# Optimization experiments

Measured on AMD Instinct MI355X. Metric: run time of the kernel, lower is better.

## Reference

```python
import jax, jax.numpy as jnp
import numpy as np

DIM = 1024
HEADS = 16

def setup_inputs() -> dict:
    key = jax.random.key(0)
    k1, k2, k3, k4 = jax.random.split(key, 4)
    x = jax.random.normal(k1, (2, 2048, DIM), dtype=jnp.float32)
    # torch Linear weights are [out_features, in_features]
    w_qkv = jax.random.normal(k2, (3 * DIM, DIM), dtype=jnp.float32) * (DIM ** -0.5)
    w_out = jax.random.normal(k3, (DIM, DIM), dtype=jnp.float32) * (DIM ** -0.5)
    b_out = jax.random.normal(k4, (DIM,), dtype=jnp.float32) * 0.01
    return {"x": x, "w_qkv": w_qkv, "w_out": w_out, "b_out": b_out}

def reference(x, w_qkv, w_out, b_out):
    b, n, dim = x.shape
    h = HEADS
    d = dim // h
    scale = dim ** -0.5  # NOTE: full dim, faithful to source
    qkv = x @ w_qkv.T                       # [b, n, 3*dim]
    qkv = qkv.reshape(b, n, 3, h, d)        # split (qkv h d)
    q, k, v = (qkv[:, :, i].transpose(0, 2, 1, 3) for i in range(3))  # [b, h, n, d]
    scores = jnp.einsum('bhid,bhjd->bhij', q, k) * scale
    weights = jax.nn.softmax(scores, axis=-1)
    out = jnp.einsum('bhij,bhjd->bhid', weights, v)  # [b, h, n, d]
    out = out.transpose(0, 2, 1, 3).reshape(b, n, dim)
    return out @ w_out.T + b_out
```

## Files before the change

kernel.cpp:

```cpp
#include <hip/hip_runtime.h>

#define DIM   1024
#define HEADS 16
#define NSEQ  2048
#define BATCH 2

typedef unsigned short u16;
typedef unsigned long long u64;
typedef __attribute__((ext_vector_type(8))) short bf16x8;
typedef __attribute__((ext_vector_type(8))) _Float16 f16x8;
typedef __attribute__((ext_vector_type(2))) __fp16 pkh2;
typedef __attribute__((ext_vector_type(4))) float f32x4;
typedef __attribute__((ext_vector_type(16))) float f32x16;

__device__ __forceinline__ u16 f2b(float f) {
  union { float f; unsigned u; } v; v.f = f;
  unsigned r = (v.u + 0x7fffu + ((v.u >> 16) & 1u)) >> 16;
  return (u16)r;
}

__device__ __forceinline__ u16 f2h(float f) {
  _Float16 h = (_Float16)f;
  return __builtin_bit_cast(u16, h);
}

__device__ __forceinline__ void g2l16(const u16* g, u16* l) {
  __builtin_amdgcn_global_load_lds(
      (const __attribute__((address_space(1))) void*)g,
      (__attribute__((address_space(3))) void*)l, 16, 0, 0);
}

__global__ void cvt_bf16(const float* __restrict__ src, u16* __restrict__ dst,
                         int n4, int sc4, float s) {
  int i = blockIdx.x * blockDim.x + threadIdx.x;
  if (i < n4) {
    float4 f = ((const float4*)src)[i];
    float m = (i < sc4) ? s : 1.0f;
    union { u16 s[4]; u64 ll; } o;
    o.s[0] = f2b(f.x * m); o.s[1] = f2b(f.y * m);
    o.s[2] = f2b(f.z * m); o.s[3] = f2b(f.w * m);
    ((u64*)dst)[i] = o.ll;
  }
}

__global__ __launch_bounds__(256, 2)
void gemm_bt(const u16* __restrict__ A, const u16* __restrict__ Bt,
             void* __restrict__ C, const float* __restrict__ bias,
             int M, int Nc, int K, int mode) {
  __shared__ u16 As[128 * 64];
  __shared__ u16 Bs[128 * 64];
  const int tid  = threadIdx.x;
  const int wave = tid >> 6, lane = tid & 63;
  const int l15  = lane & 15, quad = lane >> 4;
  const int m0 = blockIdx.y * 128, n0 = blockIdx.x * 128;
  const int wm = (wave >> 1) * 64, wn = (wave & 1) * 64;
  const int rb = wave * 32;

  f32x4 acc[4][4] = {};

  for (int kt = 0; kt < K; kt += 64) {
#pragma unroll
    for (int c = 0; c < 4; ++c) {
      int r  = rb + c * 8 + (lane >> 3);
      int ck = (lane & 7) ^ (r & 7);
      g2l16(A  + (size_t)(m0 + r) * K + kt + ck * 8, &As[(rb + c * 8) * 64]);
      g2l16(Bt + (size_t)(n0 + r) * K + kt + ck * 8, &Bs[(rb + c * 8) * 64]);
    }
    __syncthreads();
#pragma unroll
    for (int ks = 0; ks < 2; ++ks) {
      bf16x8 a[4], b[4];
      int ch = ks * 4 + quad;
#pragma unroll
      for (int i = 0; i < 4; ++i) {
        int ra  = wm + i * 16 + l15;
        a[i] = *(const bf16x8*)&As[ra * 64 + ((ch ^ (ra & 7)) << 3)];
        int rb2 = wn + i * 16 + l15;
        b[i] = *(const bf16x8*)&Bs[rb2 * 64 + ((ch ^ (rb2 & 7)) << 3)];
      }
#pragma unroll
      for (int i = 0; i < 4; ++i)
#pragma unroll
        for (int j = 0; j < 4; ++j)
          acc[i][j] = __builtin_amdgcn_mfma_f32_16x16x32_bf16(a[i], b[j], acc[i][j], 0, 0, 0);
    }
    __syncthreads();
  }

  const int as_f16 = (mode == 2) && (n0 >= 2048);
#pragma unroll
  for (int i = 0; i < 4; ++i)
#pragma unroll
    for (int j = 0; j < 4; ++j) {
      int row = m0 + wm + i * 16 + quad * 4;
      int col = n0 + wn + j * 16 + l15;
#pragma unroll
      for (int r = 0; r < 4; ++r) {
        float v = acc[i][j][r];
        if (mode == 0) ((float*)C)[(size_t)(row + r) * Nc + col] = v + bias[col];
        else ((u16*)C)[(size_t)(row + r) * Nc + col] = as_f16 ? f2h(v) : f2b(v);
      }
    }
}

__global__ __launch_bounds__(256, 2)
void attn(const u16* __restrict__ qkv, u16* __restrict__ outp) {
  __shared__ u16 Ks[2][128 * 64];
  __shared__ u16 Vts[2][64 * 128];
  const int tid  = threadIdx.x;
  const int wave = tid >> 6, lane = tid & 63;
  const int l31  = lane & 31, h = lane >> 5;
  const int b = blockIdx.x >> 4, hd = blockIdx.x & 15;
  const int q0 = blockIdx.y * 128;
  const u16* base = qkv + (size_t)b * NSEQ * 3072;
  const int qoff = hd * 64, koff = DIM + hd * 64, voff = 2 * DIM + hd * 64;
  const int dc = tid & 7, j0l = (tid >> 3) * 4;
  const int vchunk = (j0l >> 4) * 2 + ((j0l >> 2) & 1);
  const int vboff  = 4 * ((j0l >> 3) & 1);

  union V4 { uint4 q; u16 s[8]; };
  union PA { unsigned w[4]; f16x8 f; };

#pragma unroll
  for (int c = 0; c < 4; ++c) {
    int bse = wave * 32 + c * 8;
    g2l16(base + (size_t)(q0 + bse + (lane >> 3)) * 3072 + qoff + (((lane & 7) ^ ((lane >> 3) & 7)) << 3),
          &Ks[0][bse * 64]);
  }
  __syncthreads();
  bf16x8 qf[4];
  {
    int qr = wave * 32 + l31;
#pragma unroll
    for (int kd = 0; kd < 4; ++kd)
      qf[kd] = *(const bf16x8*)&Ks[0][qr * 64 + (((kd * 2 + h) ^ (qr & 7)) << 3)];
  }
  __syncthreads();

  V4 vr[4];
#pragma unroll
  for (int c = 0; c < 4; ++c) {
    int bse = wave * 32 + c * 8;
    g2l16(base + (size_t)(bse + (lane >> 3)) * 3072 + koff + (((lane & 7) ^ ((lane >> 3) & 7)) << 3),
          &Ks[0][bse * 64]);
  }
#pragma unroll
  for (int e = 0; e < 4; ++e)
    vr[e].q = *(const uint4*)(base + (size_t)(j0l + e) * 3072 + voff + dc * 8);
#pragma unroll
  for (int u = 0; u < 8; ++u) {
    int d = dc * 8 + u;
    unsigned w0 = (unsigned)vr[0].s[u] | ((unsigned)vr[1].s[u] << 16);
    unsigned w1 = (unsigned)vr[2].s[u] | ((unsigned)vr[3].s[u] << 16);
    *(u64*)&Vts[0][d * 128 + ((vchunk ^ ((d + (d >> 3)) & 15)) << 3) + vboff] =
        (u64)w0 | ((u64)w1 << 32);
  }
  __syncthreads();

  float lrun = 0.0f;
  f32x16 oacc[2] = {};

  for (int t = 0; t < 16; ++t) {
    const int pbuf = t & 1;
    if (t < 15) {
      const int j0n = (t + 1) * 128;
#pragma unroll
      for (int c = 0; c < 4; ++c) {
        int bse = wave * 32 + c * 8;
        g2l16(base + (size_t)(j0n + bse + (lane >> 3)) * 3072 + koff + (((lane & 7) ^ ((lane >> 3) & 7)) << 3),
              &Ks[pbuf ^ 1][bse * 64]);
      }
#pragma unroll
      for (int e = 0; e < 4; ++e)
        vr[e].q = *(const uint4*)(base + (size_t)(j0n + j0l + e) * 3072 + voff + dc * 8);
    }

    f32x16 sc[4] = {};
#pragma unroll
    for (int kd = 0; kd < 4; ++kd) {
      bf16x8 kb[4];
#pragma unroll
      for (int ni = 0; ni < 4; ++ni) {
        int kr = ni * 32 + l31;
        kb[ni] = *(const bf16x8*)&Ks[pbuf][kr * 64 + (((kd * 2 + h) ^ (kr & 7)) << 3)];
      }
#pragma unroll
      for (int ni = 0; ni < 4; ++ni)
        sc[ni] = __builtin_amdgcn_mfma_f32_32x32x16_bf16(kb[ni], qf[kd], sc[ni], 0, 0, 0);
    }

    PA pa[8];
#pragma unroll
    for (int ni = 0; ni < 4; ++ni) {
      f32x16 p;
#pragma unroll
      for (int r = 0; r < 16; ++r) p[r] = __builtin_amdgcn_exp2f(sc[ni][r]);
      float s0 = (p[0] + p[1]) + (p[2] + p[3]);
      float s1 = (p[4] + p[5]) + (p[6] + p[7]);
      float s2 = (p[8] + p[9]) + (p[10] + p[11]);
      float s3 = (p[12] + p[13]) + (p[14] + p[15]);
      lrun += (s0 + s1) + (s2 + s3);
#pragma unroll
      for (int ks2 = 0; ks2 < 2; ++ks2)
#pragma unroll
        for (int i = 0; i < 4; ++i) {
          pkh2 t = __builtin_amdgcn_cvt_pkrtz(p[8 * ks2 + 2 * i], p[8 * ks2 + 2 * i + 1]);
          pa[2 * ni + ks2].w[i] = __builtin_bit_cast(unsigned, t);
        }
    }

#pragma unroll
    for (int f = 0; f < 8; ++f) {
      f16x8 vb[2];
#pragma unroll
      for (int nd = 0; nd < 2; ++nd) {
        int d = nd * 32 + l31;
        vb[nd] = *(const f16x8*)&Vts[pbuf][d * 128 + (((2 * f + h) ^ ((d + (d >> 3)) & 15)) << 3)];
      }
#pragma unroll
      for (int nd = 0; nd < 2; ++nd)
        oacc[nd] = __builtin_amdgcn_mfma_f32_32x32x16_f16(pa[f].f, vb[nd], oacc[nd], 0, 0, 0);
    }

    if (t < 15) {
#pragma unroll
      for (int u = 0; u < 8; ++u) {
        int d = dc * 8 + u;
        unsigned w0 = (unsigned)vr[0].s[u] | ((unsigned)vr[1].s[u] << 16);
        unsigned w1 = (unsigned)vr[2].s[u] | ((unsigned)vr[3].s[u] << 16);
        *(u64*)&Vts[pbuf ^ 1][d * 128 + ((vchunk ^ ((d + (d >> 3)) & 15)) << 3) + vboff] =
            (u64)w0 | ((u64)w1 << 32);
      }
    }
    __syncthreads();
  }

  float linv = 1.0f / (lrun + __shfl_xor(lrun, 32, 64));
#pragma unroll
  for (int r = 0; r < 16; ++r) {
    int rowloc = (r & 3) + 8 * (r >> 2) + 4 * h;
    float lb = __shfl(linv, rowloc, 64);
    int row = q0 + wave * 32 + rowloc;
#pragma unroll
    for (int nd = 0; nd < 2; ++nd)
      outp[((size_t)b * NSEQ + row) * DIM + hd * 64 + nd * 32 + l31] = f2b(oacc[nd][r] * lb);
  }
}

extern "C" void kernel_launch(void* const* d_in, const int* in_sizes, int n_in,
                              void* d_out, int out_size, void* d_ws, size_t ws_size,
                              hipStream_t stream) {
  const float* x     = (const float*)d_in[0];
  const float* w_qkv = (const float*)d_in[1];
  const float* w_out = (const float*)d_in[2];
  const float* b_out = (const float*)d_in[3];
  float* outp = (float*)d_out;

  u16* xb    = (u16*)d_ws;
  u16* wqkvb = xb    + (size_t)4096 * 1024;
  u16* woutb = wqkvb + (size_t)3072 * 1024;
  u16* qkvb  = woutb + (size_t)1024 * 1024;
  u16* attnb = qkvb  + (size_t)4096 * 3072;

  const float C2 = 0.03125f * 1.44269504088896340736f;

  cvt_bf16<<<4096 * 1024 / 4 / 256, 256, 0, stream>>>(x,     xb,    4096 * 1024 / 4, 0, 1.0f);
  cvt_bf16<<<3072 * 1024 / 4 / 256, 256, 0, stream>>>(w_qkv, wqkvb, 3072 * 1024 / 4,
                                                      1024 * 1024 / 4, C2);
  cvt_bf16<<<1024 * 1024 / 4 / 256, 256, 0, stream>>>(w_out, woutb, 1024 * 1024 / 4, 0, 1.0f);

  gemm_bt<<<dim3(24, 32), 256, 0, stream>>>(xb, wqkvb, qkvb, nullptr, 4096, 3072, 1024, 2);
  attn<<<dim3(32, 16), 256, 0, stream>>>(qkvb, attnb);
  gemm_bt<<<dim3(8, 32), 256, 0, stream>>>(attnb, woutb, outp, b_out, 4096, 1024, 1024, 0);
}
```

Baseline: 206.9 us.

## Pre-transpose V into a global fp16 buffer and stream it directly into attention

A new kernel transposes V into a [b*h, 64, N] fp16 layout in global memory, converting it from the bf16 that the QKV GEMM now always writes. The attention kernel drops its LDS V staging, register transposes and writes, and instead loads the V operands for the PV MFMAs directly from the transposed global buffer. The score computation is also reordered into two halves of 64 keys to reduce live registers. This trades an extra kernel launch and global round-trip, plus uncached per-iteration global loads in the inner loop, for less LDS traffic and less shuffle work. V also picks up an extra rounding step, since it is now quantised to bf16 before being converted to fp16.

```diff
diff --git a/kernel.cpp b/kernel.cpp
--- a/kernel.cpp
+++ b/kernel.cpp
@@ -87,7 +87,6 @@
     __syncthreads();
   }
 
-  const int as_f16 = (mode == 2) && (n0 >= 2048);
 #pragma unroll
   for (int i = 0; i < 4; ++i)
 #pragma unroll
@@ -98,27 +97,52 @@
       for (int r = 0; r < 4; ++r) {
         float v = acc[i][j][r];
         if (mode == 0) ((float*)C)[(size_t)(row + r) * Nc + col] = v + bias[col];
-        else ((u16*)C)[(size_t)(row + r) * Nc + col] = as_f16 ? f2h(v) : f2b(v);
-      }
-    }
+        else ((u16*)C)[(size_t)(row + r) * Nc + col] = f2b(v);
+      }
+    }
+}
+
+__global__ __launch_bounds__(256)
+void vt_kernel(const u16* __restrict__ qkv, u16* __restrict__ vt) {
+  __shared__ u16 T[64][136];
+  const int tid = threadIdx.x;
+  const int bh = blockIdx.x, b = bh >> 4, h = bh & 15;
+  const int j0 = blockIdx.y * 128;
+  const u16* src = qkv + (size_t)b * NSEQ * 3072 + 2 * DIM + h * 64;
+#pragma unroll
+  for (int p = 0; p < 8; ++p) {
+    int jl = p * 16 + (tid >> 4);
+    int d0 = (tid & 15) * 4;
+    u64 v = *(const u64*)&src[(size_t)(j0 + jl) * 3072 + d0];
+#pragma unroll
+    for (int e = 0; e < 4; ++e) {
+      unsigned bf = (unsigned)((v >> (16 * e)) & 0xFFFFu) << 16;
+      T[d0 + e][jl] = f2h(__builtin_bit_cast(float, bf));
+    }
+  }
+  __syncthreads();
+  const int d = tid >> 2, g = tid & 3;
+  u16* dst = vt + ((size_t)bh * 64 + d) * NSEQ + j0 + g * 32;
+#pragma unroll
+  for (int c = 0; c < 4; ++c)
+    *(uint4*)&dst[c * 8] = *(const uint4*)&T[d][g * 32 + c * 8];
 }
 
 __global__ __launch_bounds__(256, 2)
-void attn(const u16* __restrict__ qkv, u16* __restrict__ outp) {
+void attn(const u16* __restrict__ qkv, const u16* __restrict__ vt,
+          u16* __restrict__ outp) {
   __shared__ u16 Ks[2][128 * 64];
-  __shared__ u16 Vts[2][64 * 128];
   const int tid  = threadIdx.x;
   const int wave = tid >> 6, lane = tid & 63;
   const int l31  = lane & 31, h = lane >> 5;
-  const int b = blockIdx.x >> 4, hd = blockIdx.x & 15;
+  const int bh = blockIdx.x, b = bh >> 4, hd = bh & 15;
   const int q0 = blockIdx.y * 128;
   const u16* base = qkv + (size_t)b * NSEQ * 3072;
-  const int qoff = hd * 64, koff = DIM + hd * 64, voff = 2 * DIM + hd * 64;
-  const int dc = tid & 7, j0l = (tid >> 3) * 4;
-  const int vchunk = (j0l >> 4) * 2 + ((j0l >> 2) & 1);
-  const int vboff  = 4 * ((j0l >> 3) & 1);
-
-  union V4 { uint4 q; u16 s[8]; };
+  const int qoff = hd * 64, koff = DIM + hd * 64;
+  const u16* vrow0 = vt + ((size_t)bh * 64 + l31) * NSEQ;
+  const u16* vrow1 = vrow0 + (size_t)32 * NSEQ;
+
+  union VF { u64 d[2]; f16x8 v; };
   union PA { unsigned w[4]; f16x8 f; };
 
 #pragma unroll
@@ -137,24 +161,12 @@
   }
   __syncthreads();
 
-  V4 vr[4];
 #pragma unroll
   for (int c = 0; c < 4; ++c) {
     int bse = wave * 32 + c * 8;
     g2l16(base + (size_t)(bse + (lane >> 3)) * 3072 + koff + (((lane & 7) ^ ((lane >> 3) & 7)) << 3),
           &Ks[0][bse * 64]);
   }
-#pragma unroll
-  for (int e = 0; e < 4; ++e)
-    vr[e].q = *(const uint4*)(base + (size_t)(j0l + e) * 3072 + voff + dc * 8);
-#pragma unroll
-  for (int u = 0; u < 8; ++u) {
-    int d = dc * 8 + u;
-    unsigned w0 = (unsigned)vr[0].s[u] | ((unsigned)vr[1].s[u] << 16);
-    unsigned w1 = (unsigned)vr[2].s[u] | ((unsigned)vr[3].s[u] << 16);
-    *(u64*)&Vts[0][d * 128 + ((vchunk ^ ((d + (d >> 3)) & 15)) << 3) + vboff] =
-        (u64)w0 | ((u64)w1 << 32);
-  }
   __syncthreads();
 
   float lrun = 0.0f;
@@ -170,67 +182,53 @@
         g2l16(base + (size_t)(j0n + bse + (lane >> 3)) * 3072 + koff + (((lane & 7) ^ ((lane >> 3) & 7)) << 3),
               &Ks[pbuf ^ 1][bse * 64]);
       }
-#pragma unroll
-      for (int e = 0; e < 4; ++e)
-        vr[e].q = *(const uint4*)(base + (size_t)(j0n + j0l + e) * 3072 + voff + dc * 8);
-    }
-
-    f32x16 sc[4] = {};
-#pragma unroll
-    for (int kd = 0; kd < 4; ++kd) {
-      bf16x8 kb[4];
-#pragma unroll
-      for (int ni = 0; ni < 4; ++ni) {
-        int kr = ni * 32 + l31;
-        kb[ni] = *(const bf16x8*)&Ks[pbuf][kr * 64 + (((kd * 2 + h) ^ (kr & 7)) << 3)];
-      }
-#pragma unroll
-      for (int ni = 0; ni < 4; ++ni)
-        sc[ni] = __builtin_amdgcn_mfma_f32_32x32x16_bf16(kb[ni], qf[kd], sc[ni], 0, 0, 0);
     }
 
     PA pa[8];
 #pragma unroll
-    for (int ni = 0; ni < 4; ++ni) {
-      f32x16 p;
-#pragma unroll
-      for (int r = 0; r < 16; ++r) p[r] = __builtin_amdgcn_exp2f(sc[ni][r]);
-      float s0 = (p[0] + p[1]) + (p[2] + p[3]);
-      float s1 = (p[4] + p[5]) + (p[6] + p[7]);
-      float s2 = (p[8] + p[9]) + (p[10] + p[11]);
-      float s3 = (p[12] + p[13]) + (p[14] + p[15]);
-      lrun += (s0 + s1) + (s2 + s3);
-#pragma unroll
-      for (int ks2 = 0; ks2 < 2; ++ks2)
-#pragma unroll
-        for (int i = 0; i < 4; ++i) {
-          pkh2 t = __builtin_amdgcn_cvt_pkrtz(p[8 * ks2 + 2 * i], p[8 * ks2 + 2 * i + 1]);
-          pa[2 * ni + ks2].w[i] = __builtin_bit_cast(unsigned, t);
-        }
-    }
-
+    for (int half = 0; half < 2; ++half) {
+      f32x16 s0 = {}, s1 = {};
+      const int kr0 = half * 64 + l31, kr1 = kr0 + 32;
+#pragma unroll
+      for (int kd = 0; kd < 4; ++kd) {
+        int ch = kd * 2 + h;
+        bf16x8 kb0 = *(const bf16x8*)&Ks[pbuf][kr0 * 64 + ((ch ^ (kr0 & 7)) << 3)];
+        bf16x8 kb1 = *(const bf16x8*)&Ks[pbuf][kr1 * 64 + ((ch ^ (kr1 & 7)) << 3)];
+        s0 = __builtin_amdgcn_mfma_f32_32x32x16_bf16(kb0, qf[kd], s0, 0, 0, 0);
+        s1 = __builtin_amdgcn_mfma_f32_32x32x16_bf16(kb1, qf[kd], s1, 0, 0, 0);
+      }
+#pragma unroll
+      for (int u = 0; u < 2; ++u) {
+        const f32x16& su = u ? s1 : s0;
+        f32x16 p;
+#pragma unroll
+        for (int r = 0; r < 16; ++r) p[r] = __builtin_amdgcn_exp2f(su[r]);
+        float a0 = (p[0] + p[1]) + (p[2] + p[3]);
+        float a1 = (p[4] + p[5]) + (p[6] + p[7]);
+        float a2 = (p[8] + p[9]) + (p[10] + p[11]);
+        float a3 = (p[12] + p[13]) + (p[14] + p[15]);
+        lrun += (a0 + a1) + (a2 + a3);
+#pragma unroll
+        for (int ks2 = 0; ks2 < 2; ++ks2)
+#pragma unroll
+          for (int i = 0; i < 4; ++i) {
+            pkh2 t2 = __builtin_amdgcn_cvt_pkrtz(p[8 * ks2 + 2 * i], p[8 * ks2 + 2 * i + 1]);
+            pa[4 * half + 2 * u + ks2].w[i] = __builtin_bit_cast(unsigned, t2);
+          }
+      }
+    }
+
+    const int j0 = t * 128;
 #pragma unroll
     for (int f = 0; f < 8; ++f) {
-      f16x8 vb[2];
-#pragma unroll
-      for (int nd = 0; nd < 2; ++nd) {
-        int d = nd * 32 + l31;
-        vb[nd] = *(const f16x8*)&Vts[pbuf][d * 128 + (((2 * f + h) ^ ((d + (d >> 3)) & 15)) << 3)];
-      }
-#pragma unroll
-      for (int nd = 0; nd < 2; ++nd)
-        oacc[nd] = __builtin_amdgcn_mfma_f32_32x32x16_f16(pa[f].f, vb[nd], oacc[nd], 0, 0, 0);
-    }
-
-    if (t < 15) {
-#pragma unroll
-      for (int u = 0; u < 8; ++u) {
-        int d = dc * 8 + u;
-        unsigned w0 = (unsigned)vr[0].s[u] | ((unsigned)vr[1].s[u] << 16);
-        unsigned w1 = (unsigned)vr[2].s[u] | ((unsigned)vr[3].s[u] << 16);
-        *(u64*)&Vts[pbuf ^ 1][d * 128 + ((vchunk ^ ((d + (d >> 3)) & 15)) << 3) + vboff] =
-            (u64)w0 | ((u64)w1 << 32);
-      }
+      const int off = j0 + 16 * f + 4 * h;
+      VF v0, v1;
+      v0.d[0] = *(const u64*)&vrow0[off];
+      v0.d[1] = *(const u64*)&vrow0[off + 8];
+      v1.d[0] = *(const u64*)&vrow1[off];
+      v1.d[1] = *(const u64*)&vrow1[off + 8];
+      oacc[0] = __builtin_amdgcn_mfma_f32_32x32x16_f16(pa[f].f, v0.v, oacc[0], 0, 0, 0);
+      oacc[1] = __builtin_amdgcn_mfma_f32_32x32x16_f16(pa[f].f, v1.v, oacc[1], 0, 0, 0);
     }
     __syncthreads();
   }
@@ -261,6 +259,7 @@
   u16* woutb = wqkvb + (size_t)3072 * 1024;
   u16* qkvb  = woutb + (size_t)1024 * 1024;
   u16* attnb = qkvb  + (size_t)4096 * 3072;
+  u16* vtb   = attnb + (size_t)4096 * 1024;
 
   const float C2 = 0.03125f * 1.44269504088896340736f;
 
@@ -269,7 +268,8 @@
                                                       1024 * 1024 / 4, C2);
   cvt_bf16<<<1024 * 1024 / 4 / 256, 256, 0, stream>>>(w_out, woutb, 1024 * 1024 / 4, 0, 1.0f);
 
-  gemm_bt<<<dim3(24, 32), 256, 0, stream>>>(xb, wqkvb, qkvb, nullptr, 4096, 3072, 1024, 2);
-  attn<<<dim3(32, 16), 256, 0, stream>>>(qkvb, attnb);
+  gemm_bt<<<dim3(24, 32), 256, 0, stream>>>(xb, wqkvb, qkvb, nullptr, 4096, 3072, 1024, 1);
+  vt_kernel<<<dim3(32, 16), 256, 0, stream>>>(qkvb, vtb);
+  attn<<<dim3(32, 16), 256, 0, stream>>>(qkvb, vtb, attnb);
   gemm_bt<<<dim3(8, 32), 256, 0, stream>>>(attnb, woutb, outp, b_out, 4096, 1024, 1024, 0);
 }
```

Measured after the change: 278.6 us. 34.6% more time.
